# Kernel optimization log

Hardware: AMD Instinct MI355X
Metric: run time of the kernel (lower is better)

## Reference

```python
import jax, jax.numpy as jnp
import numpy as np


def setup_inputs() -> dict:
    key = jax.random.key(0)
    ks = jax.random.split(key, 8)
    B, L, D, H, Dh = 2, 2048, 1024, 16, 64
    scale = 1.0 / np.sqrt(D)
    return {
        "inputs_q": jax.random.normal(ks[0], (B, L, D), jnp.float32),
        "inputs_kv": jax.random.normal(ks[1], (B, L, D), jnp.float32),
        "mask_k": jax.random.uniform(ks[2], (B, L), jnp.float32),
        "Wq": jax.random.normal(ks[3], (D, H, Dh), jnp.float32) * scale,
        "bq": jnp.zeros((H, Dh), jnp.float32),
        "Wk": jax.random.normal(ks[4], (D, H, Dh), jnp.float32) * scale,
        "bk": jnp.zeros((H, Dh), jnp.float32),
        "Wv": jax.random.normal(ks[5], (D, H, Dh), jnp.float32) * scale,
        "bv": jnp.zeros((H, Dh), jnp.float32),
        "Wo": jax.random.normal(ks[6], (H, Dh, D), jnp.float32) * (1.0 / np.sqrt(D)),
        "bo": jnp.zeros((D,), jnp.float32),
    }


def reference(inputs_q, inputs_kv, mask_k, Wq, bq, Wk, bk, Wv, bv, Wo, bo):
    # QKV projections: [B,L,D] x [D,H,Dh] -> [B,L,H,Dh]
    q = jnp.einsum("bld,dhk->blhk", inputs_q, Wq) + bq
    k = jnp.einsum("bld,dhk->blhk", inputs_kv, Wk) + bk
    v = jnp.einsum("bld,dhk->blhk", inputs_kv, Wv) + bv
    # vector mask applied to values per key position
    v = mask_k[:, :, None, None] * v
    head_dim = q.shape[-1]
    q = q / jnp.sqrt(jnp.asarray(head_dim, q.dtype))
    # attention scores [B,H,Lq,Lk]
    scores = jnp.einsum("bqhk,bshk->bhqs", q, k)
    probs = jax.nn.softmax(scores, axis=-1)
    # weighted values [B,Lq,H,Dh]
    x = jnp.einsum("bhqs,bshk->bqhk", probs, v)
    # output projection over (head, head_dim)
    out = jnp.einsum("bqhk,hkd->bqd", x, Wo) + bo
    return out
```

## Files before the change

### kernel.cpp

```cpp
#include <hip/hip_runtime.h>
#include <stdint.h>

typedef __attribute__((ext_vector_type(8))) short bf16x8;
typedef __attribute__((ext_vector_type(4))) float f32x4;
typedef __attribute__((ext_vector_type(16))) float f32x16;
typedef __attribute__((ext_vector_type(4))) unsigned short us4;
typedef __attribute__((ext_vector_type(4))) unsigned int u32x4;

#define AS1 __attribute__((address_space(1)))
#define AS3 __attribute__((address_space(3)))

static constexpr int Lq = 2048;
static constexpr int Dm = 1024;
static constexpr int NH = 16;
static constexpr int DH = 64;

__device__ __forceinline__ unsigned short f2bf(float x) {
  union { float f; uint32_t u; } v; v.f = x;
  uint32_t r = v.u + 0x7FFFu + ((v.u >> 16) & 1u);
  return (unsigned short)(r >> 16);
}

#if __has_builtin(__builtin_amdgcn_exp2f)
__device__ __forceinline__ float exp2_fast(float x) { return __builtin_amdgcn_exp2f(x); }
#else
__device__ __forceinline__ float exp2_fast(float x) {
  float r; asm volatile("v_exp_f32 %0, %1" : "=v"(r) : "v"(x)); return r;
}
#endif

__device__ __forceinline__ uint32_t cvtpk_bf16(float lo, float hi) {
  uint32_t r;
  asm("v_cvt_pk_bf16_f32 %0, %1, %2" : "=v"(r) : "v"(lo), "v"(hi));
  return r;
}

__device__ __forceinline__ f32x16 zero16() {
  f32x16 z;
#pragma unroll
  for (int i = 0; i < 16; ++i) z[i] = 0.f;
  return z;
}

__global__ __launch_bounds__(256) void cvt2_kernel(
    const float* __restrict__ s0, const float* __restrict__ s1,
    unsigned short* __restrict__ d0, unsigned short* __restrict__ d1, int n4) {
  const float* src = blockIdx.y ? s1 : s0;
  unsigned short* dst = blockIdx.y ? d1 : d0;
  int idx = blockIdx.x * 256 + threadIdx.x;
  int stride = gridDim.x * 256;
  for (int i = idx; i < n4; i += stride) {
    float4 f = ((const float4*)src)[i];
    us4 o = { f2bf(f.x), f2bf(f.y), f2bf(f.z), f2bf(f.w) };
    ((us4*)dst)[i] = o;
  }
}

__global__ __launch_bounds__(256) void tpose_kernel(
    const float* __restrict__ W0, const float* __restrict__ W1,
    const float* __restrict__ W2, const float* __restrict__ W3,
    unsigned short* __restrict__ T0, unsigned short* __restrict__ T1,
    unsigned short* __restrict__ T2, unsigned short* __restrict__ T3) {
  __shared__ float tile[32][33];
  const float* src; unsigned short* dst;
  switch (blockIdx.z) {
    case 0: src = W0; dst = T0; break;
    case 1: src = W1; dst = T1; break;
    case 2: src = W2; dst = T2; break;
    default: src = W3; dst = T3; break;
  }
  int x = threadIdx.x & 31, ys = threadIdx.x >> 5;
  int bx = blockIdx.x * 32, by = blockIdx.y * 32;
  for (int i = 0; i < 4; ++i) {
    int y = ys * 4 + i;
    tile[y][x] = src[(size_t)(by + y) * Dm + bx + x];
  }
  __syncthreads();
  for (int i = 0; i < 4; ++i) {
    int y = ys * 4 + i;
    dst[(size_t)(bx + y) * Dm + by + x] = f2bf(tile[x][y]);
  }
}

__global__ __launch_bounds__(256) void gemm_kernel(
    const unsigned short* __restrict__ A0, const unsigned short* __restrict__ A1,
    const unsigned short* __restrict__ W0, const unsigned short* __restrict__ W1,
    const unsigned short* __restrict__ W2,
    const float* __restrict__ b0, const float* __restrict__ b1,
    const float* __restrict__ b2, const float* __restrict__ mask,
    unsigned short* __restrict__ Qw, unsigned short* __restrict__ Kw,
    unsigned short* __restrict__ Vtw, float* __restrict__ Of, int modeBase) {
  const int mode = modeBase + blockIdx.z;
  const unsigned short* Ap = (mode == 1 || mode == 2) ? A1 : A0;
  const unsigned short* Wp = (mode == 1) ? W1 : ((mode == 2) ? W2 : W0);
  const float* bias = (mode == 1) ? b1 : ((mode == 2) ? b2 : b0);

  const int tid = threadIdx.x, lane = tid & 63, wid = tid >> 6;
  const int wm = wid >> 1, wn = wid & 1;
  const int m0 = blockIdx.x * 128, n0 = blockIdx.y * 128;
  const int ln = lane & 15, kg = lane >> 4;

  __shared__ __align__(16) unsigned short smem[24576];

  f32x4 acc[4][4];
#pragma unroll
  for (int i = 0; i < 4; ++i)
#pragma unroll
    for (int j = 0; j < 4; ++j) acc[i][j] = f32x4{0.f, 0.f, 0.f, 0.f};

  auto stage_g = [&](int buf, int k0) {
#pragma unroll
    for (int i = 0; i < 2; ++i) {
      const int t = i * 256 + tid;
      const int row = t >> 2, ch = t & 3;
      const int tb = i * 256 + wid * 64;
      __builtin_amdgcn_global_load_lds(
          (const AS1 unsigned int*)(Ap + (size_t)(m0 + row) * Dm + k0 + ch * 8),
          (AS3 unsigned int*)&smem[buf * 4096 + tb * 8], 16, 0, 0);
      __builtin_amdgcn_global_load_lds(
          (const AS1 unsigned int*)(Wp + (size_t)(n0 + row) * Dm + k0 + ch * 8),
          (AS3 unsigned int*)&smem[12288 + buf * 4096 + tb * 8], 16, 0, 0);
    }
  };
  auto comp_g = [&](int buf) {
    const unsigned short* As = &smem[buf * 4096];
    const unsigned short* Bs = &smem[12288 + buf * 4096];
    bf16x8 af[4], bfv[4];
#pragma unroll
    for (int f = 0; f < 4; ++f) {
      af[f]  = *(const bf16x8*)&As[(wm * 64 + f * 16 + ln) * 32 + kg * 8];
      bfv[f] = *(const bf16x8*)&Bs[(wn * 64 + f * 16 + ln) * 32 + kg * 8];
    }
    __builtin_amdgcn_s_setprio(1);
#pragma unroll
    for (int mf = 0; mf < 4; ++mf)
#pragma unroll
      for (int nf = 0; nf < 4; ++nf)
        acc[mf][nf] = __builtin_amdgcn_mfma_f32_16x16x32_bf16(af[mf], bfv[nf],
                                                              acc[mf][nf], 0, 0, 0);
    __builtin_amdgcn_s_setprio(0);
  };

  stage_g(0, 0);
  stage_g(1, 32);
  for (int tt = 0; tt < 30; tt += 3) {
#pragma unroll
    for (int j = 0; j < 3; ++j) {
      const int t = tt + j;
      asm volatile("s_waitcnt vmcnt(4)" ::: "memory");
      asm volatile("s_barrier" ::: "memory");
      if (t < 30) stage_g((j + 2) % 3, (t + 2) * 32);
      comp_g(j);
    }
  }
  asm volatile("s_waitcnt vmcnt(4)" ::: "memory");
  asm volatile("s_barrier" ::: "memory");
  comp_g(0);
  asm volatile("s_waitcnt vmcnt(0)" ::: "memory");
  asm volatile("s_barrier" ::: "memory");
  comp_g(1);

  __syncthreads();
  unsigned short* ep = smem + wid * 2304;
  const int rowbase = m0 + wm * 64;
  const int colbase = n0 + wn * 64;

  if (mode <= 1) {
    unsigned short* dstbase = (mode == 0) ? Qw : Kw;
    const int hh = colbase >> 6;
    const int bb_ = rowbase >> 11, lb = rowbase & 2047;
    unsigned short* dst = dstbase + ((size_t)(bb_ * NH + hh) * Lq + lb) * DH;
    const float sc = (mode == 0) ? 0.18033688f : 1.0f;
    for (int p = 0; p < 2; ++p) {
      for (int nf = 0; nf < 4; ++nf) {
        const float bv_ = bias[colbase + nf * 16 + ln];
        for (int mh = 0; mh < 2; ++mh) {
          const int mf = 2 * p + mh;
          const int rl2 = mh * 16 + kg * 4;
          for (int r = 0; r < 4; ++r)
            ep[(rl2 + r) * 72 + nf * 16 + ln] = f2bf((acc[mf][nf][r] + bv_) * sc);
        }
      }
      for (int it = 0; it < 4; ++it) {
        const int e = it * 64 + lane;
        const int rr = e >> 3, c = (e & 7) * 8;
        *(bf16x8*)(dst + (size_t)(p * 32 + rr) * DH + c) = *(const bf16x8*)&ep[rr * 72 + c];
      }
    }
  } else if (mode == 2) {
    const int hh = colbase >> 6;
    const int bb_ = rowbase >> 11;
    const int l0 = rowbase & 2047;
    unsigned short* dst = Vtw + (size_t)(bb_ * NH + hh) * DH * Lq;
    for (int p = 0; p < 2; ++p) {
      for (int nh2 = 0; nh2 < 2; ++nh2) {
        const int nf = 2 * p + nh2;
        const int dh2 = nh2 * 16 + ln;
        const float bv_ = bias[colbase + nf * 16 + ln];
        for (int mf = 0; mf < 4; ++mf)
          for (int r = 0; r < 4; ++r) {
            const int rl = mf * 16 + kg * 4 + r;
            ep[dh2 * 72 + rl] = f2bf((acc[mf][nf][r] + bv_) * mask[rowbase + rl]);
          }
      }
      for (int it = 0; it < 4; ++it) {
        const int e = it * 64 + lane;
        const int dr = e >> 3, c = (e & 7) * 8;
        *(bf16x8*)(dst + (size_t)(p * 32 + dr) * Lq + l0 + c) = *(const bf16x8*)&ep[dr * 72 + c];
      }
    }
  } else {
    float* epf = (float*)smem + wid * 1152;
    for (int mf = 0; mf < 4; ++mf) {
      for (int nf = 0; nf < 4; ++nf) {
        const float bv_ = bias[colbase + nf * 16 + ln];
        for (int r = 0; r < 4; ++r)
          epf[(kg * 4 + r) * 68 + nf * 16 + ln] = acc[mf][nf][r] + bv_;
      }
      for (int it = 0; it < 4; ++it) {
        const int e = it * 64 + lane;
        const int rr = e >> 4, c = (lane & 15) * 4;
        *(f32x4*)(Of + (size_t)(rowbase + mf * 16 + rr) * Dm + colbase + c) =
            *(const f32x4*)&epf[rr * 68 + c];
      }
    }
  }
}

__global__ __launch_bounds__(256) void attn_kernel(
    const unsigned short* __restrict__ Q, const unsigned short* __restrict__ K,
    const unsigned short* __restrict__ Vt, unsigned short* __restrict__ X) {
  const int tid = threadIdx.x, lane = tid & 63, wv = tid >> 6;
  const int lq = lane & 31, hi = lane >> 5;
  const int h = blockIdx.y, b = blockIdx.z;
  const int q0 = blockIdx.x * 128 + wv * 32;

  const size_t bh = (size_t)b * NH + h;
  const unsigned short* Qp = Q + bh * Lq * DH;
  const unsigned short* Kp = K + bh * Lq * DH;
  const unsigned short* Vp = Vt + bh * DH * Lq;

  __shared__ __align__(16) unsigned short smem[12288];
  unsigned short* Klds = smem;
  unsigned short* Vlds = smem + 6144;

  const int kr = tid >> 3, kc = tid & 7;
  const unsigned short* ksrc = Kp + (size_t)kr * DH + ((kc ^ (kr & 7)) * 8);
  const int vr = tid >> 2, vc = tid & 3;
  const unsigned short* vsrc = Vp + (size_t)vr * Lq + ((vc ^ ((vr >> 1) & 3)) * 8);

  auto stage = [&](int buf, const unsigned short* kp, const unsigned short* vp) {
    __builtin_amdgcn_global_load_lds((const AS1 unsigned int*)kp,
        (AS3 unsigned int*)&Klds[buf * 2048 + wv * 512], 16, 0, 0);
    __builtin_amdgcn_global_load_lds((const AS1 unsigned int*)vp,
        (AS3 unsigned int*)&Vlds[buf * 2048 + wv * 512], 16, 0, 0);
  };

  bf16x8 qf[4];
#pragma unroll
  for (int ks = 0; ks < 4; ++ks)
    qf[ks] = *(const bf16x8*)(Qp + (size_t)(q0 + lq) * DH + ks * 16 + hi * 8);

  f32x16 o0 = zero16(), o1 = zero16();
  float lsum = 0.f;

  auto compute = [&](const unsigned short* Kb, const unsigned short* Vb) {
    f32x16 s0 = zero16(), s1 = zero16();
    __builtin_amdgcn_s_setprio(1);
#pragma unroll
    for (int ks = 0; ks < 4; ++ks) {
      const bf16x8 kfr =
          *(const bf16x8*)&Kb[lq * 64 + (((2 * ks + hi) ^ (lq & 7)) * 8)];
      if (ks < 2) s0 = __builtin_amdgcn_mfma_f32_32x32x16_bf16(kfr, qf[ks], s0, 0, 0, 0);
      else        s1 = __builtin_amdgcn_mfma_f32_32x32x16_bf16(kfr, qf[ks], s1, 0, 0, 0);
    }
    __builtin_amdgcn_s_setprio(0);

    float p[16];
#pragma unroll
    for (int i = 0; i < 16; ++i) p[i] = exp2_fast(s0[i] + s1[i]);
    lsum += ((((p[0] + p[1]) + (p[2] + p[3])) + ((p[4] + p[5]) + (p[6] + p[7]))) +
             (((p[8] + p[9]) + (p[10] + p[11])) + ((p[12] + p[13]) + (p[14] + p[15]))));

    uint32_t a00 = cvtpk_bf16(p[0],  p[1]),  a01 = cvtpk_bf16(p[2],  p[3]);
    uint32_t a10 = cvtpk_bf16(p[4],  p[5]),  a11 = cvtpk_bf16(p[6],  p[7]);
    uint32_t a20 = cvtpk_bf16(p[8],  p[9]),  a21 = cvtpk_bf16(p[10], p[11]);
    uint32_t a30 = cvtpk_bf16(p[12], p[13]), a31 = cvtpk_bf16(p[14], p[15]);
    asm volatile("v_permlane32_swap_b32 %0, %1" : "+v"(a00), "+v"(a10));
    asm volatile("v_permlane32_swap_b32 %0, %1" : "+v"(a01), "+v"(a11));
    asm volatile("v_permlane32_swap_b32 %0, %1" : "+v"(a20), "+v"(a30));
    asm volatile("v_permlane32_swap_b32 %0, %1" : "+v"(a21), "+v"(a31));
    u32x4 pw0 = {a00, a01, a10, a11};
    u32x4 pw1 = {a20, a21, a30, a31};
    const bf16x8 pa0 = *(const bf16x8*)&pw0;
    const bf16x8 pa1 = *(const bf16x8*)&pw1;

    __builtin_amdgcn_s_setprio(1);
    {
      const int sw0 = (lq >> 1) & 3;
      const bf16x8 vb0 = *(const bf16x8*)&Vb[lq * 32 + ((hi ^ sw0) * 8)];
      const bf16x8 vb1 = *(const bf16x8*)&Vb[lq * 32 + (((2 + hi) ^ sw0) * 8)];
      o0 = __builtin_amdgcn_mfma_f32_32x32x16_bf16(pa0, vb0, o0, 0, 0, 0);
      o0 = __builtin_amdgcn_mfma_f32_32x32x16_bf16(pa1, vb1, o0, 0, 0, 0);
      const int dh1 = 32 + lq;
      const int sw1 = (dh1 >> 1) & 3;
      const bf16x8 vb2 = *(const bf16x8*)&Vb[dh1 * 32 + ((hi ^ sw1) * 8)];
      const bf16x8 vb3 = *(const bf16x8*)&Vb[dh1 * 32 + (((2 + hi) ^ sw1) * 8)];
      o1 = __builtin_amdgcn_mfma_f32_32x32x16_bf16(pa0, vb2, o1, 0, 0, 0);
      o1 = __builtin_amdgcn_mfma_f32_32x32x16_bf16(pa1, vb3, o1, 0, 0, 0);
    }
    __builtin_amdgcn_s_setprio(0);
  };

  stage(0, ksrc, vsrc);
  stage(1, ksrc + 2048, vsrc + 32);
  const unsigned short* kpre = ksrc + 4096;
  const unsigned short* vpre = vsrc + 64;
  for (int tt = 0; tt < 63; tt += 3) {
#pragma unroll
    for (int j = 0; j < 3; ++j) {
      const int t = tt + j;
      asm volatile("s_waitcnt vmcnt(2)" ::: "memory");
      asm volatile("s_barrier" ::: "memory");
      if (t < 62) {
        stage((j + 2) % 3, kpre, vpre);
        kpre += 2048; vpre += 32;
      }
      compute(&Klds[j * 2048], &Vlds[j * 2048]);
    }
  }
  asm volatile("s_waitcnt vmcnt(0)" ::: "memory");
  asm volatile("s_barrier" ::: "memory");
  compute(&Klds[0], &Vlds[0]);

  lsum += __shfl_xor(lsum, 32);
  const float inv = 1.0f / lsum;
  __syncthreads();
  unsigned short* ep = smem + wv * 2304;
#pragma unroll
  for (int r = 0; r < 16; ++r) {
    const int qrow = (r & 3) + 8 * (r >> 2) + 4 * hi;
    const float iv = __shfl(inv, qrow);
    ep[qrow * 72 + lq]      = f2bf(o0[r] * iv);
    ep[qrow * 72 + 32 + lq] = f2bf(o1[r] * iv);
  }
#pragma unroll
  for (int it = 0; it < 4; ++it) {
    const int e = it * 64 + lane;
    const int row = e >> 3, ch = e & 7;
    *(bf16x8*)(X + (size_t)(b * Lq + q0 + row) * Dm + h * DH + ch * 8) =
        *(const bf16x8*)&ep[row * 72 + ch * 8];
  }
}

extern "C" void kernel_launch(void* const* d_in, const int* in_sizes, int n_in,
                              void* d_out, int out_size, void* d_ws, size_t ws_size,
                              hipStream_t stream) {
  (void)in_sizes; (void)n_in; (void)out_size; (void)ws_size;
  const float* inputs_q  = (const float*)d_in[0];
  const float* inputs_kv = (const float*)d_in[1];
  const float* mask_k    = (const float*)d_in[2];
  const float* Wq = (const float*)d_in[3];
  const float* bq = (const float*)d_in[4];
  const float* Wk = (const float*)d_in[5];
  const float* bk = (const float*)d_in[6];
  const float* Wv = (const float*)d_in[7];
  const float* bv = (const float*)d_in[8];
  const float* Wo = (const float*)d_in[9];
  const float* bo = (const float*)d_in[10];
  float* out = (float*)d_out;

  unsigned short* ws = (unsigned short*)d_ws;
  const size_t BIG = 4194304;
  const size_t WSZ = 1048576;
  unsigned short* Xq  = ws;
  unsigned short* Xkv = Xq + BIG;
  unsigned short* Wqt = Xkv + BIG;
  unsigned short* Wkt = Wqt + WSZ;
  unsigned short* Wvt = Wkt + WSZ;
  unsigned short* Wot = Wvt + WSZ;
  unsigned short* Qw  = Wot + WSZ;
  unsigned short* Kw  = Qw + BIG;
  unsigned short* Vtw = Kw + BIG;
  unsigned short* Xat = Vtw + BIG;

  cvt2_kernel<<<dim3(512, 2), 256, 0, stream>>>(inputs_q, inputs_kv, Xq, Xkv,
                                                (int)(BIG / 4));
  tpose_kernel<<<dim3(32, 32, 4), 256, 0, stream>>>(Wq, Wk, Wv, Wo, Wqt, Wkt, Wvt, Wot);
  gemm_kernel<<<dim3(32, 8, 3), 256, 0, stream>>>(Xq, Xkv, Wqt, Wkt, Wvt, bq, bk, bv,
                                                  mask_k, Qw, Kw, Vtw, nullptr, 0);
  attn_kernel<<<dim3(16, 16, 2), 256, 0, stream>>>(Qw, Kw, Vtw, Xat);
  gemm_kernel<<<dim3(32, 8, 1), 256, 0, stream>>>(Xat, nullptr, Wot, nullptr, nullptr,
                                                  bo, nullptr, nullptr, nullptr,
                                                  nullptr, nullptr, nullptr, out, 3);
}
```

Before: 124.7 us.

## Split attention key range across two wave groups per block with LDS reduction

Doubles the attention block to 512 threads. Each half of the waves processes half of the key sequence for the same 128 queries, using its own triple-buffered LDS staging area. Partial output accumulators and row sums from the second half are reduced through shared memory before normalization and store. This raises the wave count per query tile to hide latency on a grid of only 512 blocks, at the cost of doubled LDS use, an extra reduction pass and a sync. It appears to rely on a softmax without a running max, so partial results can simply be added.

Measured after the change: 117.3 us. -5.9%, faster.

```diff
diff --git a/kernel.cpp b/kernel.cpp
--- a/kernel.cpp
+++ b/kernel.cpp
@@ -227,33 +227,35 @@
   }
 }
 
-__global__ __launch_bounds__(256) void attn_kernel(
+__global__ __launch_bounds__(512) void attn_kernel(
     const unsigned short* __restrict__ Q, const unsigned short* __restrict__ K,
     const unsigned short* __restrict__ Vt, unsigned short* __restrict__ X) {
   const int tid = threadIdx.x, lane = tid & 63, wv = tid >> 6;
   const int lq = lane & 31, hi = lane >> 5;
+  const int wq = wv & 3, half = wv >> 2;
   const int h = blockIdx.y, b = blockIdx.z;
-  const int q0 = blockIdx.x * 128 + wv * 32;
+  const int q0 = blockIdx.x * 128 + wq * 32;
 
   const size_t bh = (size_t)b * NH + h;
   const unsigned short* Qp = Q + bh * Lq * DH;
-  const unsigned short* Kp = K + bh * Lq * DH;
-  const unsigned short* Vp = Vt + bh * DH * Lq;
-
-  __shared__ __align__(16) unsigned short smem[12288];
-  unsigned short* Klds = smem;
-  unsigned short* Vlds = smem + 6144;
-
-  const int kr = tid >> 3, kc = tid & 7;
+  const unsigned short* Kp = K + bh * Lq * DH + (size_t)half * 1024 * DH;
+  const unsigned short* Vp = Vt + bh * DH * Lq + half * 1024;
+
+  __shared__ __align__(16) unsigned short smem[24576];
+  unsigned short* Klds = smem + half * 12288;
+  unsigned short* Vlds = smem + half * 12288 + 6144;
+
+  const int st = tid & 255;
+  const int kr = st >> 3, kc = st & 7;
   const unsigned short* ksrc = Kp + (size_t)kr * DH + ((kc ^ (kr & 7)) * 8);
-  const int vr = tid >> 2, vc = tid & 3;
+  const int vr = st >> 2, vc = st & 3;
   const unsigned short* vsrc = Vp + (size_t)vr * Lq + ((vc ^ ((vr >> 1) & 3)) * 8);
 
   auto stage = [&](int buf, const unsigned short* kp, const unsigned short* vp) {
     __builtin_amdgcn_global_load_lds((const AS1 unsigned int*)kp,
-        (AS3 unsigned int*)&Klds[buf * 2048 + wv * 512], 16, 0, 0);
+        (AS3 unsigned int*)&Klds[buf * 2048 + wq * 512], 16, 0, 0);
     __builtin_amdgcn_global_load_lds((const AS1 unsigned int*)vp,
-        (AS3 unsigned int*)&Vlds[buf * 2048 + wv * 512], 16, 0, 0);
+        (AS3 unsigned int*)&Vlds[buf * 2048 + wq * 512], 16, 0, 0);
   };
 
   bf16x8 qf[4];
@@ -316,40 +318,62 @@
   stage(1, ksrc + 2048, vsrc + 32);
   const unsigned short* kpre = ksrc + 4096;
   const unsigned short* vpre = vsrc + 64;
-  for (int tt = 0; tt < 63; tt += 3) {
+  for (int tt = 0; tt < 30; tt += 3) {
 #pragma unroll
     for (int j = 0; j < 3; ++j) {
-      const int t = tt + j;
       asm volatile("s_waitcnt vmcnt(2)" ::: "memory");
       asm volatile("s_barrier" ::: "memory");
-      if (t < 62) {
-        stage((j + 2) % 3, kpre, vpre);
-        kpre += 2048; vpre += 32;
-      }
+      stage((j + 2) % 3, kpre, vpre);
+      kpre += 2048; vpre += 32;
       compute(&Klds[j * 2048], &Vlds[j * 2048]);
     }
   }
+  asm volatile("s_waitcnt vmcnt(2)" ::: "memory");
+  asm volatile("s_barrier" ::: "memory");
+  compute(&Klds[0], &Vlds[0]);
   asm volatile("s_waitcnt vmcnt(0)" ::: "memory");
   asm volatile("s_barrier" ::: "memory");
-  compute(&Klds[0], &Vlds[0]);
+  compute(&Klds[2048], &Vlds[2048]);
 
   lsum += __shfl_xor(lsum, 32);
-  const float inv = 1.0f / lsum;
   __syncthreads();
-  unsigned short* ep = smem + wv * 2304;
-#pragma unroll
-  for (int r = 0; r < 16; ++r) {
-    const int qrow = (r & 3) + 8 * (r >> 2) + 4 * hi;
-    const float iv = __shfl(inv, qrow);
-    ep[qrow * 72 + lq]      = f2bf(o0[r] * iv);
-    ep[qrow * 72 + 32 + lq] = f2bf(o1[r] * iv);
-  }
-#pragma unroll
-  for (int it = 0; it < 4; ++it) {
-    const int e = it * 64 + lane;
-    const int row = e >> 3, ch = e & 7;
-    *(bf16x8*)(X + (size_t)(b * Lq + q0 + row) * Dm + h * DH + ch * 8) =
-        *(const bf16x8*)&ep[row * 72 + ch * 8];
+  float* cs = (float*)smem;
+  float* po = cs + wq * 2048;
+  float* pl = cs + 8192 + wq * 32;
+  if (half == 1) {
+#pragma unroll
+    for (int r = 0; r < 16; ++r) {
+      const int qrow = (r & 3) + 8 * (r >> 2) + 4 * hi;
+      po[qrow * 64 + lq]      = o0[r];
+      po[qrow * 64 + 32 + lq] = o1[r];
+    }
+    if (hi == 0) pl[lq] = lsum;
+  }
+  __syncthreads();
+  if (half == 0) {
+#pragma unroll
+    for (int r = 0; r < 16; ++r) {
+      const int qrow = (r & 3) + 8 * (r >> 2) + 4 * hi;
+      o0[r] += po[qrow * 64 + lq];
+      o1[r] += po[qrow * 64 + 32 + lq];
+    }
+    lsum += pl[lq];
+    const float inv = 1.0f / lsum;
+    unsigned short* ep = (unsigned short*)po;
+#pragma unroll
+    for (int r = 0; r < 16; ++r) {
+      const int qrow = (r & 3) + 8 * (r >> 2) + 4 * hi;
+      const float iv = __shfl(inv, qrow);
+      ep[qrow * 72 + lq]      = f2bf(o0[r] * iv);
+      ep[qrow * 72 + 32 + lq] = f2bf(o1[r] * iv);
+    }
+#pragma unroll
+    for (int it = 0; it < 4; ++it) {
+      const int e = it * 64 + lane;
+      const int row = e >> 3, ch = e & 7;
+      *(bf16x8*)(X + (size_t)(b * Lq + q0 + row) * Dm + h * DH + ch * 8) =
+          *(const bf16x8*)&ep[row * 72 + ch * 8];
+    }
   }
 }
 
@@ -389,7 +413,7 @@
   tpose_kernel<<<dim3(32, 32, 4), 256, 0, stream>>>(Wq, Wk, Wv, Wo, Wqt, Wkt, Wvt, Wot);
   gemm_kernel<<<dim3(32, 8, 3), 256, 0, stream>>>(Xq, Xkv, Wqt, Wkt, Wvt, bq, bk, bv,
                                                   mask_k, Qw, Kw, Vtw, nullptr, 0);
-  attn_kernel<<<dim3(16, 16, 2), 256, 0, stream>>>(Qw, Kw, Vtw, Xat);
+  attn_kernel<<<dim3(16, 16, 2), 512, 0, stream>>>(Qw, Kw, Vtw, Xat);
   gemm_kernel<<<dim3(32, 8, 1), 256, 0, stream>>>(Xat, nullptr, Wot, nullptr, nullptr,
                                                   bo, nullptr, nullptr, nullptr,
                                                   nullptr, nullptr, nullptr, out, 3);
```
